# Kernel tuning notes

Hardware: AMD Instinct MI355X
Metric: run time of the kernel (lower is better)

## Reference

```python
import jax, jax.numpy as jnp
import numpy as np

N_WIRES = 10
N_BLOCKS = 4
BATCH = 8192
FEAT = 4 * N_WIRES
DIM = 2 ** N_WIRES
BN_EPS = 1e-5

# sign of PauliZ on wire i for each basis state index (wire 0 = most significant bit,
# matching torchquantum's [bsz, 2, 2, ..., 2] state layout)
_k = np.arange(DIM)
_bits = (_k[None, :] >> (N_WIRES - 1 - np.arange(N_WIRES))[:, None]) & 1
SIGNS = jnp.asarray(1.0 - 2.0 * _bits, dtype=jnp.float32)  # [n_wires, 2^n]

H_GATE = jnp.array([[1, 1], [1, -1]], dtype=jnp.complex64) * jnp.complex64(0.70710678)
SX_GATE = jnp.complex64(0.5) * jnp.array([[1 + 1j, 1 - 1j], [1 - 1j, 1 + 1j]], dtype=jnp.complex64)


def rx_mat(theta):
    t = jnp.asarray(theta) * 0.5
    c = jnp.cos(t).astype(jnp.complex64)
    s = (-1j) * jnp.sin(t).astype(jnp.complex64)
    return jnp.stack([jnp.stack([c, s], -1), jnp.stack([s, c], -1)], -2)


def ry_mat(theta):
    t = jnp.asarray(theta) * 0.5
    c = jnp.cos(t).astype(jnp.complex64)
    s = jnp.sin(t).astype(jnp.complex64)
    return jnp.stack([jnp.stack([c, -s], -1), jnp.stack([s, c], -1)], -2)


def rz_mat(theta):
    e = jnp.exp(jnp.complex64(-0.5j) * jnp.asarray(theta).astype(jnp.complex64))
    z = jnp.zeros_like(e)
    return jnp.stack([jnp.stack([e, z], -1), jnp.stack([z, jnp.conj(e)], -1)], -2)


def apply_1q(state, gate, wire):
    # state: [B, 2, 2, ..., 2]; gate: [2,2] (shared) or [B,2,2] (per-sample encoder)
    s = jnp.moveaxis(state, wire + 1, -1)
    if gate.ndim == 3:
        s = jnp.einsum('bij,b...j->b...i', gate, s)
    else:
        s = jnp.einsum('ij,b...j->b...i', gate, s)
    return jnp.moveaxis(s, -1, wire + 1)


def apply_cnot(state, c, t):
    s = jnp.moveaxis(state, (c + 1, t + 1), (-2, -1))  # [..., ctrl, tgt]
    s = jnp.stack([s[..., 0, :], s[..., 1, ::-1]], axis=-2)
    return jnp.moveaxis(s, (-2, -1), (c + 1, t + 1))


def measure_all_z(state):
    probs = (state.real ** 2 + state.imag ** 2).reshape(state.shape[0], -1)  # [B, 2^n]
    return probs @ SIGNS.T  # [B, n_wires]


def encode(state, feats):
    # GeneralEncoder: per wire i apply rx, ry, rz, rx with data angles feats[:, 4i..4i+3]
    for i in range(N_WIRES):
        state = apply_1q(state, rx_mat(feats[:, 4 * i]), i)
        state = apply_1q(state, ry_mat(feats[:, 4 * i + 1]), i)
        state = apply_1q(state, rz_mat(feats[:, 4 * i + 2]), i)
        state = apply_1q(state, rx_mat(feats[:, 4 * i + 3]), i)
    return state


def qnn(feats, rz1, ry1, rz2, rz3):
    B = feats.shape[0]
    state = jnp.zeros((B, DIM), jnp.complex64).at[:, 0].set(1.0)
    state = state.reshape((B,) + (2,) * N_WIRES)
    for k in range(N_BLOCKS):
        for i in range(N_WIRES):
            state = apply_1q(state, rz_mat(rz1[k, i]), i)
        for i in range(N_WIRES):
            state = apply_1q(state, ry_mat(ry1[k, i]), i)
        for i in range(N_WIRES):
            state = apply_1q(state, rz_mat(rz2[k, i]), i)
        for i in range(N_WIRES):  # circular CNOT ring
            state = apply_cnot(state, i, (i + 1) % N_WIRES)
        if k != N_BLOCKS - 1:
            state = encode(state, feats)
    outs = [measure_all_z(state)]
    for i in range(N_WIRES):
        state = apply_1q(state, H_GATE, i)
    outs.append(measure_all_z(state))
    for i in range(N_WIRES):
        state = apply_1q(state, H_GATE, i)
        state = apply_1q(state, SX_GATE, i)
    outs.append(measure_all_z(state))
    for i in range(N_WIRES):  # only the last rz3 layer is applied in the source
        state = apply_1q(state, rz_mat(rz3[-1, i]), i)
    outs.append(measure_all_z(state))
    return jnp.concatenate(outs, axis=-1)  # [B, 4*n_wires]


def setup_inputs() -> dict:
    key = jax.random.key(0)
    ks = jax.random.split(key, 13)
    pi = np.float32(np.pi)
    w_scale = 1.0 / np.sqrt(np.float32(FEAT))
    return {
        'x': jax.random.normal(ks[0], (BATCH, FEAT), jnp.float32),
        'qlin_w': jax.random.normal(ks[1], (FEAT, FEAT), jnp.float32) * w_scale,
        'qlin_b': jax.random.normal(ks[2], (FEAT,), jnp.float32) * w_scale,
        'bn_gamma': jnp.ones((FEAT,), jnp.float32),
        'bn_beta': jnp.zeros((FEAT,), jnp.float32),
        'clin_w': jax.random.normal(ks[3], (FEAT, FEAT), jnp.float32) * w_scale,
        'clin_b': jax.random.normal(ks[4], (FEAT,), jnp.float32) * w_scale,
        'lin_w': jax.random.normal(ks[5], (FEAT, 2 * FEAT), jnp.float32) * w_scale,
        'lin_b': jax.random.normal(ks[6], (FEAT,), jnp.float32) * w_scale,
        'rz1': jax.random.uniform(ks[7], (N_BLOCKS, N_WIRES), jnp.float32, -pi, pi),
        'ry1': jax.random.uniform(ks[8], (N_BLOCKS, N_WIRES), jnp.float32, -pi, pi),
        'rz2': jax.random.uniform(ks[9], (N_BLOCKS, N_WIRES), jnp.float32, -pi, pi),
        'rz3': jax.random.uniform(ks[10], (N_BLOCKS, N_WIRES), jnp.float32, -pi, pi),
    }


def reference(x, qlin_w, qlin_b, bn_gamma, bn_beta, clin_w, clin_b, lin_w, lin_b, rz1, ry1, rz2, rz3):
    # quantum branch: Linear -> BatchNorm1d (training-mode batch stats) -> QNN
    xq = x @ qlin_w.T + qlin_b
    mu = xq.mean(axis=0)
    var = ((xq - mu) ** 2).mean(axis=0)  # biased variance, as torch BN
    xq = (xq - mu) * jax.lax.rsqrt(var + BN_EPS) * bn_gamma + bn_beta
    x1 = qnn(xq, rz1, ry1, rz2, rz3)
    # classical branch
    x2 = jax.nn.relu(x @ clin_w.T + clin_b)
    return jnp.concatenate([x1, x2], axis=-1) @ lin_w.T + lin_b
```

## Files before the change

kernel.cpp:

```cpp
#include <hip/hip_runtime.h>
#include <math.h>


typedef float v2f __attribute__((ext_vector_type(2)));
typedef unsigned uiv2 __attribute__((ext_vector_type(2)));

__device__ __forceinline__ float bperm1(int addr, float v){
  return __int_as_float(__builtin_amdgcn_ds_bpermute(addr, __float_as_int(v)));
}
__device__ __forceinline__ v2f bperm2(int addr, v2f v){
  v2f r; r.x = bperm1(addr, v.x); r.y = bperm1(addr, v.y); return r;
}
__device__ __forceinline__ v2f vs(float x){ return (v2f){x,x}; }

template<int C>
__device__ __forceinline__ float dppf(float x){
  return __int_as_float(__builtin_amdgcn_update_dpp(0, __float_as_int(x),
                                                    C, 0xf, 0xf, true));
}
#define QP_X1 0xB1
#define QP_X2 0x4E

__device__ __forceinline__ float xor1f(float x, int ){ return dppf<QP_X1>(x); }
__device__ __forceinline__ float xor2f(float x, int ){ return dppf<QP_X2>(x); }

__device__ __forceinline__ float xor4f(float x, int ){
  return __int_as_float(__builtin_amdgcn_ds_swizzle(__float_as_int(x), 0x101F));
}
__device__ __forceinline__ float xor8f(float x, int ){
  return __int_as_float(__builtin_amdgcn_ds_swizzle(__float_as_int(x), 0x201F));
}

#if __has_builtin(__builtin_amdgcn_permlane16_swap) && __has_builtin(__builtin_amdgcn_permlane32_swap)
__device__ __forceinline__ float xor16p(float x, int lane){
  uiv2 r = __builtin_amdgcn_permlane16_swap(__float_as_uint(x), __float_as_uint(x),
                                            false, false);
  return __uint_as_float((lane & 16) ? r.x : r.y);
}
__device__ __forceinline__ float xor32p(float x, int lane){
  uiv2 r = __builtin_amdgcn_permlane32_swap(__float_as_uint(x), __float_as_uint(x),
                                            false, false);
  return __uint_as_float((lane & 32) ? r.x : r.y);
}
#else
__device__ __forceinline__ float xor16p(float x, int lane){ return bperm1((lane^16)<<2, x); }
__device__ __forceinline__ float xor32p(float x, int lane){ return bperm1((lane^32)<<2, x); }
#endif

__device__ __forceinline__ float xor32f(float x, int a32){
  return bperm1(a32, x);
}

#define DEF_XORV(NAME, F1) \
__device__ __forceinline__ v2f NAME(v2f v, int aux){ \
  v2f r; r.x = F1(v.x,aux); r.y = F1(v.y,aux); return r; }
DEF_XORV(xor1v,   xor1f)
DEF_XORV(xor2v,   xor2f)
DEF_XORV(xor4v,   xor4f)
DEF_XORV(xor8v,   xor8f)
DEF_XORV(xor16pv, xor16p)
DEF_XORV(xor32pv, xor32p)
DEF_XORV(xor32v,  xor32f)

__device__ __forceinline__ float dsum(float x){
  x += dppf<0x111>(x);
  x += dppf<0x112>(x);
  x += dppf<0x114>(x);
  x += dppf<0x118>(x);
  x += dppf<0x142>(x);
  x += dppf<0x143>(x);
  return x;
}


#define DEF_GCROSS(NAME, PFN) \
__device__ __forceinline__ void NAME(v2f (&R)[8], v2f (&I)[8], int aux, bool hi, \
                                     const float* g){ \
  const float gar = hi ? g[6] : g[0], gai = hi ? g[7] : g[1]; \
  const float gbr = hi ? g[4] : g[2], gbi = hi ? g[5] : g[3]; \
  const v2f A=vs(gar), B=vs(gai), C=vs(gbr), D=vs(gbi); \
  _Pragma("unroll") \
  for (int c=0;c<2;++c){ \
    _Pragma("unroll") \
    for (int p=c*4;p<c*4+4;++p){ \
      v2f PR = PFN(R[p],aux); \
      v2f PI = PFN(I[p],aux); \
      v2f nr = A*R[p] - B*I[p] + C*PR - D*PI; \
      v2f ni = A*I[p] + B*R[p] + C*PI + D*PR; \
      R[p]=nr; I[p]=ni; } \
    if (c==0) __builtin_amdgcn_sched_barrier(0); \
  } \
}
DEF_GCROSS(g_cross_x32, xor32v)
DEF_GCROSS(g_cross_x16, xor16pv)
DEF_GCROSS(g_cross_x8,  xor8v)
DEF_GCROSS(g_cross_x4,  xor4v)
DEF_GCROSS(g_cross_x2,  xor2v)
DEF_GCROSS(g_cross_x1,  xor1v)

template<int PM>
__device__ __forceinline__ void g_localp(v2f (&R)[8], v2f (&I)[8], const float* g)
{
  const v2f g00r=vs(g[0]), g00i=vs(g[1]), g01r=vs(g[2]), g01i=vs(g[3]);
  const v2f g10r=vs(g[4]), g10i=vs(g[5]), g11r=vs(g[6]), g11i=vs(g[7]);
#pragma unroll
  for (int p=0;p<8;++p) if (!(p&PM)) {
    const int q = p|PM;
    v2f r0=R[p], i0=I[p], r1=R[q], i1=I[q];
    R[p] = g00r*r0 - g00i*i0 + g01r*r1 - g01i*i1;
    I[p] = g00r*i0 + g00i*r0 + g01r*i1 + g01i*r1;
    R[q] = g10r*r0 - g10i*i0 + g11r*r1 - g11i*i1;
    I[q] = g10r*i0 + g10i*r0 + g11r*i1 + g11i*r1;
  }
}

__device__ __forceinline__ void g_local9(v2f (&R)[8], v2f (&I)[8], const float* g)
{
  const v2f Gr0 = (v2f){g[0], g[4]};
  const v2f Gi0 = (v2f){g[1], g[5]};
  const v2f Gr1 = (v2f){g[2], g[6]};
  const v2f Gi1 = (v2f){g[3], g[7]};
#pragma unroll
  for (int p=0;p<8;++p) {
    v2f Rx = vs(R[p].x), Ix = vs(I[p].x);
    v2f Ry = vs(R[p].y), Iy = vs(I[p].y);
    R[p] = Gr0*Rx - Gi0*Ix + Gr1*Ry - Gi1*Iy;
    I[p] = Gr0*Ix + Gi0*Rx + Gr1*Iy + Gi1*Ry;
  }
}

__device__ __forceinline__ void cnot_ring(v2f (&R)[8], v2f (&I)[8],
                                          int addrg, int lane, bool c5)
{
#pragma unroll
  for (int p=0;p<8;++p) R[p] = bperm2(addrg, R[p]);
#pragma unroll
  for (int p=0;p<8;++p) I[p] = bperm2(addrg, I[p]);
#pragma unroll
  for (int p=0;p<4;++p) {
    v2f a=R[p], b=R[p|4];
    R[p]   = c5 ? b : a;
    R[p|4] = c5 ? a : b;
    v2f ai=I[p], bi=I[p|4];
    I[p]   = c5 ? bi : ai;
    I[p|4] = c5 ? ai : bi;
  }
#pragma unroll
  for (int p=0;p<8;++p) if ((p&4)&&!(p&2)) {
    const int q=p|2;
    v2f t=R[p]; R[p]=R[q]; R[q]=t;
    t=I[p]; I[p]=I[q]; I[q]=t;
  }
#pragma unroll
  for (int p=0;p<8;++p) if ((p&2)&&!(p&1)) {
    const int q=p|1;
    v2f t=R[p]; R[p]=R[q]; R[q]=t;
    t=I[p]; I[p]=I[q]; I[q]=t;
  }
#pragma unroll
  for (int p=1;p<8;p+=2) {
    R[p] = __builtin_shufflevector(R[p],R[p],1,0);
    I[p] = __builtin_shufflevector(I[p],I[p],1,0);
  }
#pragma unroll
  for (int p=0;p<8;++p) {
    R[p].y = xor32p(R[p].y, lane);
    I[p].y = xor32p(I[p].y, lane);
  }
}

__global__ __launch_bounds__(256) void k_pre(const float* __restrict__ x,
    const float* __restrict__ qw, const float* __restrict__ qb,
    float* __restrict__ ps)
{
  const int f = blockIdx.x >> 3, slice = blockIdx.x & 7;
  const int t = threadIdx.x;
  __shared__ float wf[40];
  __shared__ float a1[4], a2[4];
  if (t < 40) wf[t] = qw[f*40 + t];
  __syncthreads();
  const float bf = qb[f];
  float s1 = 0.f, s2 = 0.f;
#pragma unroll
  for (int i = 0; i < 4; ++i) {
    const int s = slice*1024 + t + i*256;
    const float4* xr = (const float4*)(x + s*40);
    float d = bf;
#pragma unroll
    for (int q = 0; q < 10; ++q) {
      float4 v = xr[q];
      d = fmaf(v.x, wf[4*q+0], d);
      d = fmaf(v.y, wf[4*q+1], d);
      d = fmaf(v.z, wf[4*q+2], d);
      d = fmaf(v.w, wf[4*q+3], d);
    }
    s1 += d; s2 = fmaf(d, d, s2);
  }
  s1 = dsum(s1); s2 = dsum(s2);
  const int lane = t & 63, wid = t >> 6;
  if (lane == 63) { a1[wid] = s1; a2[wid] = s2; }
  __syncthreads();
  if (t == 0) {
    ps[blockIdx.x*2+0] = a1[0]+a1[1]+a1[2]+a1[3];
    ps[blockIdx.x*2+1] = a2[0]+a2[1]+a2[2]+a2[3];
  }
}


#define GEN10(PTR) \
  g_cross_x32(R,I,a32,h0,(PTR)+0);   g_cross_x16(R,I,lane,h1,(PTR)+8);  \
  g_cross_x8 (R,I,0,h2,(PTR)+16);    g_cross_x4 (R,I,0,h3,(PTR)+24); \
  g_cross_x2 (R,I,0,h4,(PTR)+32);    g_cross_x1 (R,I,0,h5,(PTR)+40); \
  g_localp<4>(R,I,(PTR)+48);   g_localp<2>(R,I,(PTR)+56);   \
  g_localp<1>(R,I,(PTR)+64);   g_local9(R,I,(PTR)+72);

__global__ __launch_bounds__(256) void k_qnn(const float* __restrict__ x,
    const float* __restrict__ qlin_w, const float* __restrict__ qlin_b,
    const float* __restrict__ ps,
    const float* __restrict__ gamma, const float* __restrict__ beta,
    const float* __restrict__ rz1, const float* __restrict__ ry1,
    const float* __restrict__ rz2,
    const float* __restrict__ clin_w, const float* __restrict__ clin_b,
    const float* __restrict__ lin_w, const float* __restrict__ lin_b,
    float* __restrict__ out)
{
  const int tix  = threadIdx.x;
  const int lane = tix & 63;
  const int wv   = tix >> 6;

  __shared__ float Gbuf[40][8];
  __shared__ float bnA[40], bnC[40];
  __shared__ float Ebuf[4][10][8];
  __shared__ float Fbuf[4][3][10][8];
  __shared__ float xs [4][40];
  __shared__ float xqs[4][40];
  __shared__ float x1s[4][40];
  __shared__ float x2s[4][40];

  if (tix < 160) xs[tix/40][tix%40] = x[blockIdx.x*160 + tix];
  if (tix >= 160 && tix < 200) {
    const int gi = tix - 160;
    float g = rz1[gi], ay = ry1[gi], bz = rz2[gi];
    float ha = 0.5f*ay, hp = 0.5f*(bz+g), hm = 0.5f*(bz-g);
    float ca = __cosf(ha), sa = __sinf(ha);
    float cp = __cosf(hp), sp = __sinf(hp);
    float cm = __cosf(hm), sm = __sinf(hm);
    float* G = &Gbuf[gi][0];
    G[0]= ca*cp; G[1]=-ca*sp;
    G[2]=-sa*cm; G[3]= sa*sm;
    G[4]= sa*cm; G[5]= sa*sm;
    G[6]= ca*cp; G[7]= ca*sp;
  }
  if (tix >= 200 && tix < 240) {
    const int f = tix - 200;
    float s1 = 0.f, s2 = 0.f;
#pragma unroll
    for (int k = 0; k < 8; ++k) {
      s1 += ps[(f*8+k)*2+0];
      s2 += ps[(f*8+k)*2+1];
    }
    float mu  = s1 * (1.f/8192.f);
    float var = s2 * (1.f/8192.f) - mu*mu;
    float a = gamma[f] * rsqrtf(var + 1e-5f);
    bnA[f] = a; bnC[f] = beta[f] - mu*a;
  }
  __syncthreads();

  if (tix < 160) {
    const int sl = tix/40, f = tix - sl*40;
    const float4* qw = (const float4*)(qlin_w + f*40);
    float acc = qlin_b[f];
#pragma unroll
    for (int q = 0; q < 10; ++q) {
      float4 v = qw[q];
      acc = fmaf(v.x, xs[sl][4*q+0], acc);
      acc = fmaf(v.y, xs[sl][4*q+1], acc);
      acc = fmaf(v.z, xs[sl][4*q+2], acc);
      acc = fmaf(v.w, xs[sl][4*q+3], acc);
    }
    xqs[sl][f] = acc;
  }
  __syncthreads();

  if (lane < 10) {
    const int i = lane;
    const int f = 4*i;
    float a0 = 0.5f * fmaf(xqs[wv][f+0], bnA[f+0], bnC[f+0]);
    float a1 = 0.5f * fmaf(xqs[wv][f+1], bnA[f+1], bnC[f+1]);
    float a2 = 0.5f * fmaf(xqs[wv][f+2], bnA[f+2], bnC[f+2]);
    float a3 = 0.5f * fmaf(xqs[wv][f+3], bnA[f+3], bnC[f+3]);
    float c0 = __cosf(a0), s0 = __sinf(a0);
    float c1 = __cosf(a1), s1 = __sinf(a1);
    float c2 = __cosf(a2), s2 = __sinf(a2);
    float c3 = __cosf(a3), s3 = __sinf(a3);
    float A00r=c1*c0, A00i= s1*s0;
    float A01r=-s1*c0, A01i=-c1*s0;
    float A10r= s1*c0, A10i=-c1*s0;
    float A11r= c1*c0, A11i=-s1*s0;
    float B00r = A00r*c2 + A00i*s2, B00i = A00i*c2 - A00r*s2;
    float B01r = A01r*c2 + A01i*s2, B01i = A01i*c2 - A01r*s2;
    float B10r = A10r*c2 - A10i*s2, B10i = A10i*c2 + A10r*s2;
    float B11r = A11r*c2 - A11i*s2, B11i = A11i*c2 + A11r*s2;
    float* e = &Ebuf[wv][i][0];
    e[0] = c3*B00r + s3*B10i;  e[1] = c3*B00i - s3*B10r;
    e[2] = c3*B01r + s3*B11i;  e[3] = c3*B01i - s3*B11r;
    e[4] = c3*B10r + s3*B00i;  e[5] = c3*B10i - s3*B00r;
    e[6] = c3*B11r + s3*B01i;  e[7] = c3*B11i - s3*B01r;
  }

  if (lane < 30) {
    const int k = lane/10, i = lane - k*10;
    const float* U = &Gbuf[(k+1)*10 + i][0];
    const float* E = &Ebuf[wv][i][0];
    float u00r=U[0],u00i=U[1],u01r=U[2],u01i=U[3],u10r=U[4],u10i=U[5],u11r=U[6],u11i=U[7];
    float e00r=E[0],e00i=E[1],e01r=E[2],e01i=E[3],e10r=E[4],e10i=E[5],e11r=E[6],e11i=E[7];
    float* F = &Fbuf[wv][k][i][0];
    F[0] = u00r*e00r - u00i*e00i + u01r*e10r - u01i*e10i;
    F[1] = u00r*e00i + u00i*e00r + u01r*e10i + u01i*e10r;
    F[2] = u00r*e01r - u00i*e01i + u01r*e11r - u01i*e11i;
    F[3] = u00r*e01i + u00i*e01r + u01r*e11i + u01i*e11r;
    F[4] = u10r*e00r - u10i*e00i + u11r*e10r - u11i*e10i;
    F[5] = u10r*e00i + u10i*e00r + u11r*e10i + u11i*e10r;
    F[6] = u10r*e01r - u10i*e01i + u11r*e11r - u11i*e11i;
    F[7] = u10r*e01i + u10i*e01r + u11r*e11i + u11i*e11r;
  }

  const bool h0 = (lane & 32) != 0;
  const bool h1 = (lane & 16) != 0;
  const bool h2 = (lane &  8) != 0;
  const bool h3 = (lane &  4) != 0;
  const bool h4 = (lane &  2) != 0;
  const bool h5 = (lane &  1) != 0;
  const int addrg = (lane ^ (lane >> 1)) << 2;
  const int a32   = (lane ^ 32) << 2;

  v2f R[8], I[8];
  {
    const int l0=lane&1, l1=(lane>>1)&1, l2=(lane>>2)&1,
              l3=(lane>>3)&1, l4=(lane>>4)&1, l5=(lane>>5)&1;
    float csr, csi;
    {
      int b = l3^l4; csr = Gbuf[2][4*b]; csi = Gbuf[2][4*b+1];
      b = l2^l3; float gr=Gbuf[3][4*b], gi=Gbuf[3][4*b+1];
      float tr = csr*gr - csi*gi, ti = csr*gi + csi*gr; csr=tr; csi=ti;
      b = l1^l2; gr=Gbuf[4][4*b]; gi=Gbuf[4][4*b+1];
      tr = csr*gr - csi*gi; ti = csr*gi + csi*gr; csr=tr; csi=ti;
      b = l0^l1; gr=Gbuf[5][4*b]; gi=Gbuf[5][4*b+1];
      tr = csr*gr - csi*gi; ti = csr*gi + csi*gr; csr=tr; csi=ti;
    }
    float cer,cei,cor_,coi;
    {
      const int b5 = l5, b4 = l4^l5;
      float ar = Gbuf[0][4*b5],     ai = Gbuf[0][4*b5+1];
      float br = Gbuf[1][4*b4],     bi = Gbuf[1][4*b4+1];
      float tr = ar*br - ai*bi,     ti = ar*bi + ai*br;
      cer = tr*csr - ti*csi;  cei = tr*csi + ti*csr;
      ar = Gbuf[0][4*(1^b5)]; ai = Gbuf[0][4*(1^b5)+1];
      br = Gbuf[1][4*(1^b4)]; bi = Gbuf[1][4*(1^b4)+1];
      tr = ar*br - ai*bi;     ti = ar*bi + ai*br;
      cor_ = tr*csr - ti*csi; coi = tr*csi + ti*csr;
    }
    float p67r[4], p67i[4], p89r[4], p89i[4];
#pragma unroll
    for (int b6=0;b6<2;++b6)
#pragma unroll
      for (int b7=0;b7<2;++b7) {
        const float x6r = Gbuf[6][4*b6], x6i = Gbuf[6][4*b6+1];
        const float x7r = Gbuf[7][4*b7], x7i = Gbuf[7][4*b7+1];
        p67r[b6*2+b7] = x6r*x7r - x6i*x7i;
        p67i[b6*2+b7] = x6r*x7i + x6i*x7r;
      }
#pragma unroll
    for (int b8=0;b8<2;++b8)
#pragma unroll
      for (int b9=0;b9<2;++b9) {
        const float x8r = Gbuf[8][4*b8], x8i = Gbuf[8][4*b8+1];
        const float x9r = Gbuf[9][4*b9], x9i = Gbuf[9][4*b9+1];
        p89r[b8*2+b9] = x8r*x9r - x8i*x9i;
        p89i[b8*2+b9] = x8r*x9i + x8i*x9r;
      }
#pragma unroll
    for (int p=0;p<8;++p) {
      const int b3 = (p>>2)&1, b2 = (p>>1)&1, b1 = p&1;
      const int i67 = ((b3 ^ l0) << 1) | (b2 ^ b3);
      const int b1p = b1 ^ b2;
      const int ix  = (b1p<<1) | b1;
      const int iy  = (b1p<<1) | (1^b1);
      const float ter  = cer*p67r[i67] - cei*p67i[i67];
      const float tei  = cer*p67i[i67] + cei*p67r[i67];
      const float tor_ = cor_*p67r[i67] - coi*p67i[i67];
      const float toi  = cor_*p67i[i67] + coi*p67r[i67];
      R[p].x = ter*p89r[ix] - tei*p89i[ix];
      I[p].x = ter*p89i[ix] + tei*p89r[ix];
      R[p].y = tor_*p89r[iy] - toi*p89i[iy];
      I[p].y = tor_*p89i[iy] + toi*p89r[iy];
    }
  }

  { const float* F = &Fbuf[wv][0][0][0]; GEN10(F) }
  cnot_ring(R,I,addrg,lane,h5);
  { const float* F = &Fbuf[wv][1][0][0]; GEN10(F) }
  cnot_ring(R,I,addrg,lane,h5);
  { const float* F = &Fbuf[wv][2][0][0]; GEN10(F) }
  cnot_ring(R,I,addrg,lane,h5);

  float* dst = &x1s[wv][0];

  {
    v2f T8 = vs(0.f);
    v2f aa[4];
#pragma unroll
    for (int m=0;m<4;++m) aa[m] = vs(0.f);
#pragma unroll
    for (int p=0;p<8;++p) {
      v2f t = R[p]*R[p] + I[p]*I[p];
      T8 = (p&1) ? (T8 - t) : (T8 + t);
      aa[p>>1] += t;
    }
    v2f T7 = (aa[0]-aa[1]) + (aa[2]-aa[3]);
    v2f T6 = (aa[0]+aa[1]) - (aa[2]+aa[3]);
    v2f S  = (aa[0]+aa[1]) + (aa[2]+aa[3]);
    float q8 = T8.x + T8.y;
    float q7 = T7.x + T7.y;
    float q6 = T6.x + T6.y;
    float q9 = S.x - S.y;
    float P  = S.x + S.y;

    float v = P;
    { float pt = xor1f (v,0);    v = h5 ? (pt - v) : (pt + v); }
    { float pt = xor2f (v,0);    v = h4 ? (pt - v) : (pt + v); }
    { float pt = xor4f (v,0);    v = h3 ? (pt - v) : (pt + v); }
    { float pt = xor8f (v,0);    v = h2 ? (pt - v) : (pt + v); }
    { float pt = xor16p(v,lane); v = h1 ? (pt - v) : (pt + v); }
    { float pt = xor32p(v,lane); v = h0 ? (pt - v) : (pt + v); }

    q6 = dsum(q6); q7 = dsum(q7); q8 = dsum(q8); q9 = dsum(q9);

    if (lane==32) dst[0]=v;
    if (lane==16) dst[1]=v;
    if (lane== 8) dst[2]=v;
    if (lane== 4) dst[3]=v;
    if (lane== 2) dst[4]=v;
    if (lane== 1) dst[5]=v;
    if (lane==63){ dst[6]=q6; dst[7]=q7; dst[8]=q8; dst[9]=q9; }
  }

#define XYC(PFN,AUX,HW,W) { \
    v2f U=vs(0.f), V=vs(0.f); \
    _Pragma("unroll") \
    for (int c=0;c<2;++c){ \
      _Pragma("unroll") \
      for (int p=c*4;p<c*4+4;++p) { \
        v2f PR = PFN(R[p],AUX); \
        v2f PI = PFN(I[p],AUX); \
        U += R[p]*PR + I[p]*PI; \
        V += I[p]*PR - R[p]*PI; \
      } \
      if (c==0) __builtin_amdgcn_sched_barrier(0); \
    } \
    float u = U.x + U.y; \
    float vv = V.x + V.y; \
    vv = (HW) ? vv : -vv; \
    u = dsum(u); vv = dsum(vv); \
    if (lane==63){ dst[10+(W)]=u; dst[20+(W)]=vv; dst[30+(W)]=vv; } \
  }
  XYC(xor32pv,lane,h0,0) XYC(xor16pv,lane,h1,1) XYC(xor8v,0,h2,2)
  XYC(xor4v ,0,h3,3) XYC(xor2v ,0,h4,4) XYC(xor1v,0,h5,5)
#undef XYC

#define XYL(PM,W) { \
    v2f U=vs(0.f), V=vs(0.f); \
    _Pragma("unroll") \
    for (int p=0;p<8;++p) if (!(p&(PM))) { \
      const int q=p|(PM); \
      U += R[p]*R[q] + I[p]*I[q]; \
      V += I[p]*R[q] - R[p]*I[q]; \
    } \
    float u = U.x + U.y; \
    float vv = V.x + V.y; \
    u = dsum(u); vv = dsum(vv); \
    if (lane==63){ dst[10+(W)]=2.f*u; float y=-2.f*vv; dst[20+(W)]=y; dst[30+(W)]=y; } \
  }
  XYL(4,6) XYL(2,7) XYL(1,8)
#undef XYL

  {
    float u=0.f, vv=0.f;
#pragma unroll
    for (int p=0;p<8;++p) {
      u  = fmaf(R[p].x, R[p].y, u);  u  = fmaf(I[p].x, I[p].y, u);
      vv = fmaf(I[p].x, R[p].y, vv); vv = fmaf(-R[p].x, I[p].y, vv);
    }
    u = dsum(u); vv = dsum(vv);
    if (lane==63){ dst[19]=2.f*u; float y=-2.f*vv; dst[29]=y; dst[39]=y; }
  }

  __syncthreads();
  if (tix < 160) {
    const int sl = tix/40, f = tix - sl*40;
    const float4* cw = (const float4*)(clin_w + f*40);
    float acc = clin_b[f];
#pragma unroll
    for (int q = 0; q < 10; ++q) {
      float4 v = cw[q];
      acc = fmaf(v.x, xs[sl][4*q+0], acc);
      acc = fmaf(v.y, xs[sl][4*q+1], acc);
      acc = fmaf(v.z, xs[sl][4*q+2], acc);
      acc = fmaf(v.w, xs[sl][4*q+3], acc);
    }
    x2s[sl][f] = fmaxf(acc, 0.f);
  }
  __syncthreads();
  if (tix < 160) {
    const int sl = tix/40, f = tix - sl*40;
    const float4* lw = (const float4*)(lin_w + f*80);
    float o = lin_b[f];
#pragma unroll
    for (int q = 0; q < 10; ++q) {
      float4 v = lw[q];
      o = fmaf(v.x, x1s[sl][4*q+0], o);
      o = fmaf(v.y, x1s[sl][4*q+1], o);
      o = fmaf(v.z, x1s[sl][4*q+2], o);
      o = fmaf(v.w, x1s[sl][4*q+3], o);
    }
#pragma unroll
    for (int q = 10; q < 20; ++q) {
      float4 v = lw[q];
      o = fmaf(v.x, x2s[sl][4*(q-10)+0], o);
      o = fmaf(v.y, x2s[sl][4*(q-10)+1], o);
      o = fmaf(v.z, x2s[sl][4*(q-10)+2], o);
      o = fmaf(v.w, x2s[sl][4*(q-10)+3], o);
    }
    out[blockIdx.x*160 + tix] = o;
  }
}

extern "C" void kernel_launch(void* const* d_in, const int* in_sizes, int n_in,
                              void* d_out, int out_size, void* d_ws, size_t ws_size,
                              hipStream_t stream)
{
  const float* x      = (const float*)d_in[0];
  const float* qlin_w = (const float*)d_in[1];
  const float* qlin_b = (const float*)d_in[2];
  const float* bn_g   = (const float*)d_in[3];
  const float* bn_b   = (const float*)d_in[4];
  const float* clin_w = (const float*)d_in[5];
  const float* clin_b = (const float*)d_in[6];
  const float* lin_w  = (const float*)d_in[7];
  const float* lin_b  = (const float*)d_in[8];
  const float* rz1    = (const float*)d_in[9];
  const float* ry1    = (const float*)d_in[10];
  const float* rz2    = (const float*)d_in[11];

  float* ps  = (float*)d_ws;
  float* out = (float*)d_out;

  hipLaunchKernelGGL(k_pre, dim3(320),  dim3(256), 0, stream, x, qlin_w, qlin_b, ps);
  hipLaunchKernelGGL(k_qnn, dim3(2048), dim3(256), 0, stream,
                     x, qlin_w, qlin_b, ps, bn_g, bn_b, rz1, ry1, rz2,
                     clin_w, clin_b, lin_w, lin_b, out);
}
```

Before: 159.6 us.

## Use one 64-thread block per sample instead of four samples per block

Shrinks the QNN kernel from 256-thread blocks handling four samples (one wavefront each) to 64-thread blocks handling a single sample, launching 8192 blocks. The aim is to drop the barriers shared across four wavefronts, so each wavefront no longer waits on the others, and to lower shared-memory use per block. In exchange, per-block setup (gate matrices, BN coefficients from partial sums) is now computed four times as often, and the 40-lane linear stages run on a single wave with the rest of its lanes idle.

Measured after the change: 161.8 us. About the same (+1.4%).

```diff
diff --git a/kernel.cpp b/kernel.cpp
--- a/kernel.cpp
+++ b/kernel.cpp
@@ -214,7 +214,7 @@
   g_localp<4>(R,I,(PTR)+48);   g_localp<2>(R,I,(PTR)+56);   \
   g_localp<1>(R,I,(PTR)+64);   g_local9(R,I,(PTR)+72);
 
-__global__ __launch_bounds__(256) void k_qnn(const float* __restrict__ x,
+__global__ __launch_bounds__(64) void k_qnn(const float* __restrict__ x,
     const float* __restrict__ qlin_w, const float* __restrict__ qlin_b,
     const float* __restrict__ ps,
     const float* __restrict__ gamma, const float* __restrict__ beta,
@@ -224,71 +224,67 @@
     const float* __restrict__ lin_w, const float* __restrict__ lin_b,
     float* __restrict__ out)
 {
-  const int tix  = threadIdx.x;
-  const int lane = tix & 63;
-  const int wv   = tix >> 6;
+  const int lane = threadIdx.x;
+  const int smp  = blockIdx.x;
 
   __shared__ float Gbuf[40][8];
   __shared__ float bnA[40], bnC[40];
-  __shared__ float Ebuf[4][10][8];
-  __shared__ float Fbuf[4][3][10][8];
-  __shared__ float xs [4][40];
-  __shared__ float xqs[4][40];
-  __shared__ float x1s[4][40];
-  __shared__ float x2s[4][40];
-
-  if (tix < 160) xs[tix/40][tix%40] = x[blockIdx.x*160 + tix];
-  if (tix >= 160 && tix < 200) {
-    const int gi = tix - 160;
-    float g = rz1[gi], ay = ry1[gi], bz = rz2[gi];
+  __shared__ float Ebuf[10][8];
+  __shared__ float Fbuf[3][10][8];
+  __shared__ float xs [40];
+  __shared__ float xqs[40];
+  __shared__ float x1s[40];
+  __shared__ float x2s[40];
+
+  if (lane < 40) {
+    xs[lane] = x[smp*40 + lane];
+
+    float g = rz1[lane], ay = ry1[lane], bz = rz2[lane];
     float ha = 0.5f*ay, hp = 0.5f*(bz+g), hm = 0.5f*(bz-g);
     float ca = __cosf(ha), sa = __sinf(ha);
     float cp = __cosf(hp), sp = __sinf(hp);
     float cm = __cosf(hm), sm = __sinf(hm);
-    float* G = &Gbuf[gi][0];
+    float* G = &Gbuf[lane][0];
     G[0]= ca*cp; G[1]=-ca*sp;
     G[2]=-sa*cm; G[3]= sa*sm;
     G[4]= sa*cm; G[5]= sa*sm;
     G[6]= ca*cp; G[7]= ca*sp;
-  }
-  if (tix >= 200 && tix < 240) {
-    const int f = tix - 200;
+
     float s1 = 0.f, s2 = 0.f;
 #pragma unroll
     for (int k = 0; k < 8; ++k) {
-      s1 += ps[(f*8+k)*2+0];
-      s2 += ps[(f*8+k)*2+1];
+      s1 += ps[(lane*8+k)*2+0];
+      s2 += ps[(lane*8+k)*2+1];
     }
     float mu  = s1 * (1.f/8192.f);
     float var = s2 * (1.f/8192.f) - mu*mu;
-    float a = gamma[f] * rsqrtf(var + 1e-5f);
-    bnA[f] = a; bnC[f] = beta[f] - mu*a;
+    float a = gamma[lane] * rsqrtf(var + 1e-5f);
+    bnA[lane] = a; bnC[lane] = beta[lane] - mu*a;
   }
   __syncthreads();
 
-  if (tix < 160) {
-    const int sl = tix/40, f = tix - sl*40;
-    const float4* qw = (const float4*)(qlin_w + f*40);
-    float acc = qlin_b[f];
+  if (lane < 40) {
+    const float4* qw = (const float4*)(qlin_w + lane*40);
+    float acc = qlin_b[lane];
 #pragma unroll
     for (int q = 0; q < 10; ++q) {
       float4 v = qw[q];
-      acc = fmaf(v.x, xs[sl][4*q+0], acc);
-      acc = fmaf(v.y, xs[sl][4*q+1], acc);
-      acc = fmaf(v.z, xs[sl][4*q+2], acc);
-      acc = fmaf(v.w, xs[sl][4*q+3], acc);
-    }
-    xqs[sl][f] = acc;
+      acc = fmaf(v.x, xs[4*q+0], acc);
+      acc = fmaf(v.y, xs[4*q+1], acc);
+      acc = fmaf(v.z, xs[4*q+2], acc);
+      acc = fmaf(v.w, xs[4*q+3], acc);
+    }
+    xqs[lane] = acc;
   }
   __syncthreads();
 
   if (lane < 10) {
     const int i = lane;
     const int f = 4*i;
-    float a0 = 0.5f * fmaf(xqs[wv][f+0], bnA[f+0], bnC[f+0]);
-    float a1 = 0.5f * fmaf(xqs[wv][f+1], bnA[f+1], bnC[f+1]);
-    float a2 = 0.5f * fmaf(xqs[wv][f+2], bnA[f+2], bnC[f+2]);
-    float a3 = 0.5f * fmaf(xqs[wv][f+3], bnA[f+3], bnC[f+3]);
+    float a0 = 0.5f * fmaf(xqs[f+0], bnA[f+0], bnC[f+0]);
+    float a1 = 0.5f * fmaf(xqs[f+1], bnA[f+1], bnC[f+1]);
+    float a2 = 0.5f * fmaf(xqs[f+2], bnA[f+2], bnC[f+2]);
+    float a3 = 0.5f * fmaf(xqs[f+3], bnA[f+3], bnC[f+3]);
     float c0 = __cosf(a0), s0 = __sinf(a0);
     float c1 = __cosf(a1), s1 = __sinf(a1);
     float c2 = __cosf(a2), s2 = __sinf(a2);
@@ -301,7 +297,7 @@
     float B01r = A01r*c2 + A01i*s2, B01i = A01i*c2 - A01r*s2;
     float B10r = A10r*c2 - A10i*s2, B10i = A10i*c2 + A10r*s2;
     float B11r = A11r*c2 - A11i*s2, B11i = A11i*c2 + A11r*s2;
-    float* e = &Ebuf[wv][i][0];
+    float* e = &Ebuf[i][0];
     e[0] = c3*B00r + s3*B10i;  e[1] = c3*B00i - s3*B10r;
     e[2] = c3*B01r + s3*B11i;  e[3] = c3*B01i - s3*B11r;
     e[4] = c3*B10r + s3*B00i;  e[5] = c3*B10i - s3*B00r;
@@ -311,10 +307,10 @@
   if (lane < 30) {
     const int k = lane/10, i = lane - k*10;
     const float* U = &Gbuf[(k+1)*10 + i][0];
-    const float* E = &Ebuf[wv][i][0];
+    const float* E = &Ebuf[i][0];
     float u00r=U[0],u00i=U[1],u01r=U[2],u01i=U[3],u10r=U[4],u10i=U[5],u11r=U[6],u11i=U[7];
     float e00r=E[0],e00i=E[1],e01r=E[2],e01i=E[3],e10r=E[4],e10i=E[5],e11r=E[6],e11i=E[7];
-    float* F = &Fbuf[wv][k][i][0];
+    float* F = &Fbuf[k][i][0];
     F[0] = u00r*e00r - u00i*e00i + u01r*e10r - u01i*e10i;
     F[1] = u00r*e00i + u00i*e00r + u01r*e10i + u01i*e10r;
     F[2] = u00r*e01r - u00i*e01i + u01r*e11r - u01i*e11i;
@@ -397,14 +393,14 @@
     }
   }
 
-  { const float* F = &Fbuf[wv][0][0][0]; GEN10(F) }
+  { const float* F = &Fbuf[0][0][0]; GEN10(F) }
   cnot_ring(R,I,addrg,lane,h5);
-  { const float* F = &Fbuf[wv][1][0][0]; GEN10(F) }
+  { const float* F = &Fbuf[1][0][0]; GEN10(F) }
   cnot_ring(R,I,addrg,lane,h5);
-  { const float* F = &Fbuf[wv][2][0][0]; GEN10(F) }
+  { const float* F = &Fbuf[2][0][0]; GEN10(F) }
   cnot_ring(R,I,addrg,lane,h5);
 
-  float* dst = &x1s[wv][0];
+  float* dst = &x1s[0];
 
   {
     v2f T8 = vs(0.f);
@@ -496,42 +492,40 @@
   }
 
   __syncthreads();
-  if (tix < 160) {
-    const int sl = tix/40, f = tix - sl*40;
-    const float4* cw = (const float4*)(clin_w + f*40);
-    float acc = clin_b[f];
+  if (lane < 40) {
+    const float4* cw = (const float4*)(clin_w + lane*40);
+    float acc = clin_b[lane];
 #pragma unroll
     for (int q = 0; q < 10; ++q) {
       float4 v = cw[q];
-      acc = fmaf(v.x, xs[sl][4*q+0], acc);
-      acc = fmaf(v.y, xs[sl][4*q+1], acc);
-      acc = fmaf(v.z, xs[sl][4*q+2], acc);
-      acc = fmaf(v.w, xs[sl][4*q+3], acc);
-    }
-    x2s[sl][f] = fmaxf(acc, 0.f);
+      acc = fmaf(v.x, xs[4*q+0], acc);
+      acc = fmaf(v.y, xs[4*q+1], acc);
+      acc = fmaf(v.z, xs[4*q+2], acc);
+      acc = fmaf(v.w, xs[4*q+3], acc);
+    }
+    x2s[lane] = fmaxf(acc, 0.f);
   }
   __syncthreads();
-  if (tix < 160) {
-    const int sl = tix/40, f = tix - sl*40;
-    const float4* lw = (const float4*)(lin_w + f*80);
-    float o = lin_b[f];
+  if (lane < 40) {
+    const float4* lw = (const float4*)(lin_w + lane*80);
+    float o = lin_b[lane];
 #pragma unroll
     for (int q = 0; q < 10; ++q) {
       float4 v = lw[q];
-      o = fmaf(v.x, x1s[sl][4*q+0], o);
-      o = fmaf(v.y, x1s[sl][4*q+1], o);
-      o = fmaf(v.z, x1s[sl][4*q+2], o);
-      o = fmaf(v.w, x1s[sl][4*q+3], o);
+      o = fmaf(v.x, x1s[4*q+0], o);
+      o = fmaf(v.y, x1s[4*q+1], o);
+      o = fmaf(v.z, x1s[4*q+2], o);
+      o = fmaf(v.w, x1s[4*q+3], o);
     }
 #pragma unroll
     for (int q = 10; q < 20; ++q) {
       float4 v = lw[q];
-      o = fmaf(v.x, x2s[sl][4*(q-10)+0], o);
-      o = fmaf(v.y, x2s[sl][4*(q-10)+1], o);
-      o = fmaf(v.z, x2s[sl][4*(q-10)+2], o);
-      o = fmaf(v.w, x2s[sl][4*(q-10)+3], o);
-    }
-    out[blockIdx.x*160 + tix] = o;
+      o = fmaf(v.x, x2s[4*(q-10)+0], o);
+      o = fmaf(v.y, x2s[4*(q-10)+1], o);
+      o = fmaf(v.z, x2s[4*(q-10)+2], o);
+      o = fmaf(v.w, x2s[4*(q-10)+3], o);
+    }
+    out[smp*40 + lane] = o;
   }
 }
 
@@ -556,7 +550,7 @@
   float* out = (float*)d_out;
 
   hipLaunchKernelGGL(k_pre, dim3(320),  dim3(256), 0, stream, x, qlin_w, qlin_b, ps);
-  hipLaunchKernelGGL(k_qnn, dim3(2048), dim3(256), 0, stream,
+  hipLaunchKernelGGL(k_qnn, dim3(8192), dim3(64), 0, stream,
                      x, qlin_w, qlin_b, ps, bn_g, bn_b, rz1, ry1, rz2,
                      clin_w, clin_b, lin_w, lin_b, out);
 }
```
